# Kernel optimization log

Hardware: AMD Instinct MI355X
Metric: run time of the kernel (lower is better)

## Reference

```python
import jax, jax.numpy as jnp
import numpy as np

D = 1024
B, LQ, LK = 8, 2048, 2048
NEG = -1e9


def setup_inputs() -> dict:
    key = jax.random.key(0)
    ks = jax.random.split(key, 8)
    query = jax.random.normal(ks[0], (B, LQ, D), dtype=jnp.float32)
    k_in = jax.random.normal(ks[1], (B, LK, D), dtype=jnp.float32)
    value = jax.random.normal(ks[2], (B, LK, D), dtype=jnp.float32)
    mask = jax.random.randint(ks[3], (B, LK), 0, 2, dtype=jnp.int32)
    s = 1.0 / np.sqrt(D)
    Wq_w = jax.random.normal(ks[4], (D, D), dtype=jnp.float32) * s
    Wq_b = jnp.zeros((D,), dtype=jnp.float32)
    Wk_w = jax.random.normal(ks[5], (D, D), dtype=jnp.float32) * s
    Wk_b = jnp.zeros((D,), dtype=jnp.float32)
    return {"query": query, "key": k_in, "value": value, "mask": mask,
            "Wq_w": Wq_w, "Wq_b": Wq_b, "Wk_w": Wk_w, "Wk_b": Wk_b}


def reference(query, key, value, mask, Wq_w, Wq_b, Wk_w, Wk_b):
    # Linear projections (torch Linear: x @ W.T + b)
    q = jnp.einsum('bld,ed->ble', query, Wq_w) + Wq_b  # [B, Lq, D]
    k = jnp.einsum('bld,ed->ble', key, Wk_w) + Wk_b    # [B, Lk, D]
    scale = 1.0 / jnp.sqrt(jnp.asarray(D, dtype=q.dtype))
    aw = jnp.einsum('bqd,bkd->bqk', q, k) * scale      # [B, Lq, Lk]
    # custom multiplicative + additive masking: mask -> [B, 1, Lk]
    m = mask.astype(aw.dtype)[:, None, :]
    aw = aw * m
    aw = jnp.where(m == 0, jnp.asarray(NEG, dtype=aw.dtype), aw)
    attn = jax.nn.softmax(aw, axis=-1)
    return jnp.einsum('bqk,bkd->bqd', attn, value)     # [B, Lq, D]
```

## Files before the change

kernel.cpp:

```cpp
#include <hip/hip_runtime.h>

typedef __bf16 bf16;
typedef __bf16 bf16x8 __attribute__((ext_vector_type(8)));
typedef float f32x4 __attribute__((ext_vector_type(4)));
typedef float f32x16 __attribute__((ext_vector_type(16)));

__device__ __forceinline__ void gl_lds16(const bf16* g, bf16* l) {
  __builtin_amdgcn_global_load_lds(
      (__attribute__((address_space(1))) void*)g,
      (__attribute__((address_space(3))) void*)l, 16, 0, 0);
}

__global__ __launch_bounds__(256) void cvt_f32_bf16(
    const float* __restrict__ src, bf16* __restrict__ dst, int n8) {
  int i = blockIdx.x * 256 + threadIdx.x;
  if (i >= n8) return;
  const float4* s4 = (const float4*)src;
  float4 a = s4[2 * i], b = s4[2 * i + 1];
  bf16x8 o = {(bf16)a.x, (bf16)a.y, (bf16)a.z, (bf16)a.w,
              (bf16)b.x, (bf16)b.y, (bf16)b.z, (bf16)b.w};
  *(bf16x8*)(dst + (size_t)i * 8) = o;
}

__global__ __launch_bounds__(256) void transpose_v(
    const float* __restrict__ V, bf16* __restrict__ VT) {
  int b = blockIdx.z;
  const float* Vb = V + (size_t)b * 2048 * 1024;
  bf16* Tb = VT + (size_t)b * 1024 * 2048;
  __shared__ float tile[32][33];
  int tx = threadIdx.x, ty = threadIdx.y;
  int x = blockIdx.x * 32 + tx;
  int yb = blockIdx.y * 32;
#pragma unroll
  for (int j = 0; j < 4; j++)
    tile[ty + j * 8][tx] = Vb[(size_t)(yb + ty + j * 8) * 1024 + x];
  __syncthreads();
  int xo = yb + tx;
#pragma unroll
  for (int j = 0; j < 4; j++)
    Tb[(size_t)(blockIdx.x * 32 + ty + j * 8) * 2048 + xo] =
        (bf16)tile[tx][ty + j * 8];
}

template <int MODE>
__global__ __launch_bounds__(512, 2) void gemm256(
    const bf16* __restrict__ A, const bf16* __restrict__ Bm,
    void* __restrict__ Cv, const float* __restrict__ bias,
    const int* __restrict__ mask, int M, int N, int K,
    long long sA, long long sB, long long sC) {
  const int b = blockIdx.z;
  const bf16* Ab = A + (long long)b * sA;
  const bf16* Bb = Bm + (long long)b * sB;

  const int nx = gridDim.x, nwg = nx * gridDim.y;
  const int orig = blockIdx.y * nx + blockIdx.x;
  const int swz = (orig & 7) * (nwg >> 3) + (orig >> 3);
  const int m0 = (swz / nx) * 256, n0 = (swz % nx) * 256;

  __shared__ __align__(16) bf16 lds[4][2][256 * 32];

  const int tid = threadIdx.x, w = tid >> 6, lane = tid & 63;
  const int wr = w >> 2, wc = w & 3;
  const int fr = lane & 31;
  const int fh = lane >> 5;
  const int key = lane & 3;
  const bf16* Aq = Ab + (long long)m0 * K;
  const bf16* Bq = Bb + (long long)n0 * K;

  f32x16 acc[4][2];
#pragma unroll
  for (int i = 0; i < 4; i++)
#pragma unroll
    for (int j = 0; j < 2; j++)
#pragma unroll
      for (int r = 0; r < 16; r++) acc[i][j][r] = 0.f;

  const int srow = lane >> 2;
  const int sgsw = ((lane & 3) ^ (srow & 3)) * 8;
  auto stage_part = [&](int t, int p) {
    const int rg = t & 3;
    const int row = p * 128 + w * 16 + srow;
    const long long gc = (long long)t * 32 + sgsw;
    const int dbase = (p * 128 + w * 16) * 32;
    gl_lds16(Aq + (long long)row * K + gc, &lds[rg][0][dbase]);
    gl_lds16(Bq + (long long)row * K + gc, &lds[rg][1][dbase]);
  };

  auto do_slice = [&](int s, bool stg) {
    const int rg = s & 3;
    bf16x8 af[4][2], bfr[2];
#pragma unroll
    for (int mi = 0; mi < 4; mi++)
#pragma unroll
      for (int ks = 0; ks < 2; ks++) {
        const int row = wr * 128 + mi * 32 + fr;
        const int slot = (ks * 2 + fh) ^ key;
        af[mi][ks] = *(const bf16x8*)&lds[rg][0][row * 32 + slot * 8];
      }
#pragma unroll
    for (int ks = 0; ks < 2; ks++) {
      const int row = wc * 64 + fr;
      const int slot = (ks * 2 + fh) ^ key;
      bfr[ks] = *(const bf16x8*)&lds[rg][1][row * 32 + slot * 8];
    }
    if (stg) stage_part(s + 3, 0);
    __builtin_amdgcn_s_setprio(1);
#pragma unroll
    for (int mi = 0; mi < 4; mi++)
#pragma unroll
      for (int ks = 0; ks < 2; ks++)
        acc[mi][0] = __builtin_amdgcn_mfma_f32_32x32x16_bf16(
            af[mi][ks], bfr[ks], acc[mi][0], 0, 0, 0);
    __builtin_amdgcn_s_setprio(0);
#pragma unroll
    for (int ks = 0; ks < 2; ks++) {
      const int row = wc * 64 + 32 + fr;
      const int slot = (ks * 2 + fh) ^ key;
      bfr[ks] = *(const bf16x8*)&lds[rg][1][row * 32 + slot * 8];
    }
    if (stg) stage_part(s + 3, 1);
    __builtin_amdgcn_s_setprio(1);
#pragma unroll
    for (int mi = 0; mi < 4; mi++)
#pragma unroll
      for (int ks = 0; ks < 2; ks++)
        acc[mi][1] = __builtin_amdgcn_mfma_f32_32x32x16_bf16(
            af[mi][ks], bfr[ks], acc[mi][1], 0, 0, 0);
    __builtin_amdgcn_s_setprio(0);
  };

  const int NS = K >> 5;
  stage_part(0, 0); stage_part(0, 1);
  stage_part(1, 0); stage_part(1, 1);
  stage_part(2, 0); stage_part(2, 1);

  for (int s = 0; s < NS - 2; ++s) {
    asm volatile("s_waitcnt vmcnt(8)" ::: "memory");
    __builtin_amdgcn_s_barrier();
    do_slice(s, s + 3 < NS);
  }
  asm volatile("s_waitcnt vmcnt(4)" ::: "memory");
  __builtin_amdgcn_s_barrier();
  do_slice(NS - 2, false);
  asm volatile("s_waitcnt vmcnt(0)" ::: "memory");
  __builtin_amdgcn_s_barrier();
  do_slice(NS - 1, false);

  const int ecol = lane & 31, er4 = (lane >> 5) * 4;
  if constexpr (MODE == 0) {
    bf16* C = (bf16*)Cv;
#pragma unroll
    for (int ni = 0; ni < 2; ni++) {
      int col = n0 + wc * 64 + ni * 32 + ecol;
      float bv = bias[col];
#pragma unroll
      for (int mi = 0; mi < 4; mi++)
#pragma unroll
        for (int r = 0; r < 16; r++) {
          int row = m0 + wr * 128 + mi * 32 + er4 + (r & 3) + 8 * (r >> 2);
          C[(long long)row * N + col] = (bf16)(acc[mi][ni][r] + bv);
        }
    }
  } else if constexpr (MODE == 1) {
    bf16* C = (bf16*)Cv + (long long)b * sC;
    const int* mb = mask + b * 2048;
#pragma unroll
    for (int ni = 0; ni < 2; ni++) {
      int col = n0 + wc * 64 + ni * 32 + ecol;
      bool keep = mb[col] != 0;
#pragma unroll
      for (int mi = 0; mi < 4; mi++)
#pragma unroll
        for (int r = 0; r < 16; r++) {
          int row = m0 + wr * 128 + mi * 32 + er4 + (r & 3) + 8 * (r >> 2);
          C[(long long)row * N + col] =
              keep ? (bf16)(acc[mi][ni][r] * 0.03125f) : (bf16)(-1e9f);
        }
    }
  } else {
    float* C = (float*)Cv + (long long)b * sC;
#pragma unroll
    for (int ni = 0; ni < 2; ni++) {
      int col = n0 + wc * 64 + ni * 32 + ecol;
#pragma unroll
      for (int mi = 0; mi < 4; mi++)
#pragma unroll
        for (int r = 0; r < 16; r++) {
          int row = m0 + wr * 128 + mi * 32 + er4 + (r & 3) + 8 * (r >> 2);
          C[(long long)row * N + col] = acc[mi][ni][r];
        }
    }
  }
}

__global__ __launch_bounds__(256) void softmax_rows(
    const bf16* __restrict__ S, bf16* __restrict__ P) {
  long long row = blockIdx.x;
  const bf16x8* src = (const bf16x8*)(S + row * 2048);
  int tid = threadIdx.x, w = tid >> 6, lane = tid & 63;
  bf16x8 v = src[tid];
  float f[8];
#pragma unroll
  for (int i = 0; i < 8; i++) f[i] = (float)v[i];
  float m = f[0];
#pragma unroll
  for (int i = 1; i < 8; i++) m = fmaxf(m, f[i]);
#pragma unroll
  for (int off = 32; off; off >>= 1) m = fmaxf(m, __shfl_xor(m, off, 64));
  __shared__ float redm[4], reds[4];
  if (lane == 0) redm[w] = m;
  __syncthreads();
  m = fmaxf(fmaxf(redm[0], redm[1]), fmaxf(redm[2], redm[3]));
  float e[8], s = 0.f;
#pragma unroll
  for (int i = 0; i < 8; i++) {
    e[i] = __expf(f[i] - m);
    s += e[i];
  }
#pragma unroll
  for (int off = 32; off; off >>= 1) s += __shfl_xor(s, off, 64);
  if (lane == 0) reds[w] = s;
  __syncthreads();
  s = reds[0] + reds[1] + reds[2] + reds[3];
  float inv = 1.0f / s;
  bf16x8 o;
#pragma unroll
  for (int i = 0; i < 8; i++) o[i] = (bf16)(e[i] * inv);
  *(bf16x8*)(P + row * 2048 + tid * 8) = o;
}

extern "C" void kernel_launch(void* const* d_in, const int* in_sizes, int n_in,
                              void* d_out, int out_size, void* d_ws,
                              size_t ws_size, hipStream_t stream) {
  const float* query = (const float*)d_in[0];
  const float* key_in = (const float*)d_in[1];
  const float* value = (const float*)d_in[2];
  const int* mask = (const int*)d_in[3];
  const float* Wq_w = (const float*)d_in[4];
  const float* Wq_b = (const float*)d_in[5];
  const float* Wk_w = (const float*)d_in[6];
  const float* Wk_b = (const float*)d_in[7];
  float* out = (float*)d_out;

  const size_t MB = 1ull << 20;
  char* base = (char*)d_ws;
  bf16* qx = (bf16*)(base + 0 * MB);
  bf16* kx = (bf16*)(base + 32 * MB);
  bf16* wq = (bf16*)(base + 64 * MB);
  bf16* wk = (bf16*)(base + 66 * MB);
  bf16* S = (bf16*)(base + 0 * MB);
  bf16* qp = (bf16*)(base + 128 * MB);
  bf16* kp = (bf16*)(base + 160 * MB);
  bf16* P = (bf16*)(base + 128 * MB);
  bf16* vt = (bf16*)(base + 192 * MB);

  cvt_f32_bf16<<<8192, 256, 0, stream>>>(query, qx, 2097152);
  cvt_f32_bf16<<<8192, 256, 0, stream>>>(key_in, kx, 2097152);
  cvt_f32_bf16<<<512, 256, 0, stream>>>(Wq_w, wq, 131072);
  cvt_f32_bf16<<<512, 256, 0, stream>>>(Wk_w, wk, 131072);
  transpose_v<<<dim3(32, 64, 8), dim3(32, 8), 0, stream>>>(value, vt);

  gemm256<0><<<dim3(4, 64, 1), 512, 0, stream>>>(
      qx, wq, qp, Wq_b, nullptr, 16384, 1024, 1024, 0, 0, 0);
  gemm256<0><<<dim3(4, 64, 1), 512, 0, stream>>>(
      kx, wk, kp, Wk_b, nullptr, 16384, 1024, 1024, 0, 0, 0);
  gemm256<1><<<dim3(8, 8, 8), 512, 0, stream>>>(
      qp, kp, S, nullptr, mask, 2048, 2048, 1024, 2048LL * 1024,
      2048LL * 1024, 2048LL * 2048);
  softmax_rows<<<16384, 256, 0, stream>>>(S, P);
  gemm256<2><<<dim3(4, 8, 8), 512, 0, stream>>>(
      P, vt, out, nullptr, nullptr, 2048, 1024, 2048, 2048LL * 2048,
      1024LL * 2048, 2048LL * 1024);
}
```

Before: 506.5 us.

## Switch GEMM main loop to double-buffered BK=64 tiles

Replaces the 4-stage ring of 32-wide K slices with a 2-buffer pipeline of 64-wide K tiles. The next tile is prefetched before the current one is computed, and each tile is separated by two barriers. The XOR swizzle widens to 8 slots to match the 64-column rows. This halves the number of loop iterations and barrier waits per K, and issues all 8 MFMAs per k-step from the same fragment loads. In exchange it shortens prefetch depth to one tile ahead and adds a second barrier per iteration, which may expose load latency.

```diff
diff --git a/kernel.cpp b/kernel.cpp
--- a/kernel.cpp
+++ b/kernel.cpp
@@ -57,13 +57,13 @@
   const int swz = (orig & 7) * (nwg >> 3) + (orig >> 3);
   const int m0 = (swz / nx) * 256, n0 = (swz % nx) * 256;
 
-  __shared__ __align__(16) bf16 lds[4][2][256 * 32];
+  __shared__ __align__(16) bf16 lds[2][2][256 * 64];
 
   const int tid = threadIdx.x, w = tid >> 6, lane = tid & 63;
   const int wr = w >> 2, wc = w & 3;
   const int fr = lane & 31;
   const int fh = lane >> 5;
-  const int key = lane & 3;
+  const int key = lane & 7;
   const bf16* Aq = Ab + (long long)m0 * K;
   const bf16* Bq = Bb + (long long)n0 * K;
 
@@ -75,76 +75,58 @@
 #pragma unroll
       for (int r = 0; r < 16; r++) acc[i][j][r] = 0.f;
 
-  const int srow = lane >> 2;
-  const int sgsw = ((lane & 3) ^ (srow & 3)) * 8;
-  auto stage_part = [&](int t, int p) {
-    const int rg = t & 3;
-    const int row = p * 128 + w * 16 + srow;
-    const long long gc = (long long)t * 32 + sgsw;
-    const int dbase = (p * 128 + w * 16) * 32;
-    gl_lds16(Aq + (long long)row * K + gc, &lds[rg][0][dbase]);
-    gl_lds16(Bq + (long long)row * K + gc, &lds[rg][1][dbase]);
+  const int srow = lane >> 3;
+  const int sgsw = ((lane & 7) ^ srow) * 8;
+  auto stage_tile = [&](int t) {
+    const int buf = t & 1;
+    const long long gc = (long long)t * 64 + sgsw;
+    const int r0 = w * 8 + srow;
+#pragma unroll
+    for (int p = 0; p < 4; p++) {
+      const long long r = p * 64 + r0;
+      const int dbase = (p * 64 + w * 8) * 64;
+      gl_lds16(Aq + r * K + gc, &lds[buf][0][dbase]);
+      gl_lds16(Bq + r * K + gc, &lds[buf][1][dbase]);
+    }
   };
 
-  auto do_slice = [&](int s, bool stg) {
-    const int rg = s & 3;
-    bf16x8 af[4][2], bfr[2];
-#pragma unroll
-    for (int mi = 0; mi < 4; mi++)
-#pragma unroll
-      for (int ks = 0; ks < 2; ks++) {
-        const int row = wr * 128 + mi * 32 + fr;
-        const int slot = (ks * 2 + fh) ^ key;
-        af[mi][ks] = *(const bf16x8*)&lds[rg][0][row * 32 + slot * 8];
-      }
-#pragma unroll
-    for (int ks = 0; ks < 2; ks++) {
-      const int row = wc * 64 + fr;
-      const int slot = (ks * 2 + fh) ^ key;
-      bfr[ks] = *(const bf16x8*)&lds[rg][1][row * 32 + slot * 8];
-    }
-    if (stg) stage_part(s + 3, 0);
-    __builtin_amdgcn_s_setprio(1);
-#pragma unroll
-    for (int mi = 0; mi < 4; mi++)
-#pragma unroll
-      for (int ks = 0; ks < 2; ks++)
-        acc[mi][0] = __builtin_amdgcn_mfma_f32_32x32x16_bf16(
-            af[mi][ks], bfr[ks], acc[mi][0], 0, 0, 0);
-    __builtin_amdgcn_s_setprio(0);
-#pragma unroll
-    for (int ks = 0; ks < 2; ks++) {
-      const int row = wc * 64 + 32 + fr;
-      const int slot = (ks * 2 + fh) ^ key;
-      bfr[ks] = *(const bf16x8*)&lds[rg][1][row * 32 + slot * 8];
-    }
-    if (stg) stage_part(s + 3, 1);
-    __builtin_amdgcn_s_setprio(1);
-#pragma unroll
-    for (int mi = 0; mi < 4; mi++)
-#pragma unroll
-      for (int ks = 0; ks < 2; ks++)
-        acc[mi][1] = __builtin_amdgcn_mfma_f32_32x32x16_bf16(
-            af[mi][ks], bfr[ks], acc[mi][1], 0, 0, 0);
-    __builtin_amdgcn_s_setprio(0);
+  auto compute_tile = [&](int buf) {
+    const bf16* la = &lds[buf][0][0];
+    const bf16* lb = &lds[buf][1][0];
+#pragma unroll
+    for (int kk = 0; kk < 4; kk++) {
+      const int slot = ((kk * 2 + fh) ^ key) * 8;
+      bf16x8 af[4], bfr[2];
+#pragma unroll
+      for (int mi = 0; mi < 4; mi++)
+        af[mi] = *(const bf16x8*)&la[(wr * 128 + mi * 32 + fr) * 64 + slot];
+#pragma unroll
+      for (int ni = 0; ni < 2; ni++)
+        bfr[ni] = *(const bf16x8*)&lb[(wc * 64 + ni * 32 + fr) * 64 + slot];
+      __builtin_amdgcn_s_setprio(1);
+#pragma unroll
+      for (int mi = 0; mi < 4; mi++)
+#pragma unroll
+        for (int ni = 0; ni < 2; ni++)
+          acc[mi][ni] = __builtin_amdgcn_mfma_f32_32x32x16_bf16(
+              af[mi], bfr[ni], acc[mi][ni], 0, 0, 0);
+      __builtin_amdgcn_s_setprio(0);
+    }
   };
 
-  const int NS = K >> 5;
-  stage_part(0, 0); stage_part(0, 1);
-  stage_part(1, 0); stage_part(1, 1);
-  stage_part(2, 0); stage_part(2, 1);
-
-  for (int s = 0; s < NS - 2; ++s) {
-    asm volatile("s_waitcnt vmcnt(8)" ::: "memory");
+  const int NT = K >> 6;
+  stage_tile(0);
+  for (int t = 0; t < NT; ++t) {
+    if (t + 1 < NT) {
+      stage_tile(t + 1);
+      asm volatile("s_waitcnt vmcnt(8)" ::: "memory");
+    } else {
+      asm volatile("s_waitcnt vmcnt(0)" ::: "memory");
+    }
     __builtin_amdgcn_s_barrier();
-    do_slice(s, s + 3 < NS);
+    compute_tile(t & 1);
+    __builtin_amdgcn_s_barrier();
   }
-  asm volatile("s_waitcnt vmcnt(4)" ::: "memory");
-  __builtin_amdgcn_s_barrier();
-  do_slice(NS - 2, false);
-  asm volatile("s_waitcnt vmcnt(0)" ::: "memory");
-  __builtin_amdgcn_s_barrier();
-  do_slice(NS - 1, false);
 
   const int ecol = lane & 31, er4 = (lane >> 5) * 4;
   if constexpr (MODE == 0) {
```

Result: faster. 492.5 us (-2.8%).
